# Kernel optimization log

Hardware: AMD Instinct MI355X
Metric: run time of the kernel (lower is better)

The kernel has to match this reference:

```python
import jax, jax.numpy as jnp
import numpy as np

MEM_DIM = 1024
N_CHILD = 16384

def _linear_params(key, out_dim, in_dim):
    kw, kb = jax.random.split(key)
    bound = 1.0 / np.sqrt(in_dim)
    W = jax.random.uniform(kw, (out_dim, in_dim), jnp.float32, -bound, bound)
    b = jax.random.uniform(kb, (out_dim,), jnp.float32, -bound, bound)
    return W, b

def setup_inputs() -> dict:
    key = jax.random.key(0)
    ks = jax.random.split(key, 7)
    child_c = jax.random.normal(ks[0], (N_CHILD, MEM_DIM), jnp.float32)
    child_h = jax.random.normal(ks[1], (N_CHILD, MEM_DIM), jnp.float32)
    child_h_sum = jax.random.normal(ks[2], (MEM_DIM,), jnp.float32)
    W_ih, b_ih = _linear_params(ks[3], MEM_DIM, MEM_DIM)
    W_fh, b_fh = _linear_params(ks[4], MEM_DIM, MEM_DIM)
    W_uh, b_uh = _linear_params(ks[5], MEM_DIM, MEM_DIM)
    W_oh, b_oh = _linear_params(ks[6], MEM_DIM, MEM_DIM)
    return {
        "child_c": child_c, "child_h": child_h, "child_h_sum": child_h_sum,
        "W_ih": W_ih, "b_ih": b_ih, "W_fh": W_fh, "b_fh": b_fh,
        "W_uh": W_uh, "b_uh": b_uh, "W_oh": W_oh, "b_oh": b_oh,
    }

def reference(child_c, child_h, child_h_sum,
              W_ih, b_ih, W_fh, b_fh, W_uh, b_uh, W_oh, b_oh):
    # Gate projections on the summed child hidden state: [mem_dim]
    i = jax.nn.sigmoid(child_h_sum @ W_ih.T + b_ih)
    o = jax.nn.sigmoid(child_h_sum @ W_oh.T + b_oh)
    u = jnp.tanh(child_h_sum @ W_uh.T + b_uh)
    # Per-child forget gates, batched (replaces the Python loop): [N, mem_dim]
    f = jax.nn.sigmoid(child_h @ W_fh.T + b_fh)
    fc = f * child_c                     # [N, mem_dim]
    c = i * u + jnp.sum(fc, axis=0)      # [mem_dim]
    h = o * jnp.tanh(c)                  # [mem_dim]
    return (c, h)
```

## Files before the change

### kernel.cpp

```cpp
#include <hip/hip_runtime.h>
#include <hip/hip_bf16.h>
#include <math.h>

#define MEM_DIM 1024
#define N_CHILD 16384

#define BM 128
#define BN 64
#define BK 128
#define KITERS (MEM_DIM / BK)

typedef __bf16 bf16_t;
typedef __bf16 bf16x4 __attribute__((ext_vector_type(4)));
typedef __bf16 bf16x8 __attribute__((ext_vector_type(8)));
typedef float f32x4 __attribute__((ext_vector_type(4)));

__device__ __forceinline__ void async_load16(const bf16_t* g, bf16_t* l) {
    __builtin_amdgcn_global_load_lds(
        (const __attribute__((address_space(1))) unsigned int*)g,
        (__attribute__((address_space(3))) unsigned int*)l,
        16, 0, 0);
}

__global__ __launch_bounds__(256) void prep_kernel(
        const float* __restrict__ child_h, const float* __restrict__ W_fh,
        bf16_t* __restrict__ dst, int n8,
        const float* __restrict__ hsum,
        const float* __restrict__ W_ih, const float* __restrict__ b_ih,
        const float* __restrict__ W_uh, const float* __restrict__ b_uh,
        const float* __restrict__ W_oh, const float* __restrict__ b_oh,
        float* __restrict__ acc_c, float* __restrict__ o_ws) {
    const int tid = threadIdx.x;
    if (blockIdx.x < MEM_DIM) {
        const int j = blockIdx.x;
        const float* wi = W_ih + (size_t)j * MEM_DIM;
        const float* wu = W_uh + (size_t)j * MEM_DIM;
        const float* wo = W_oh + (size_t)j * MEM_DIM;
        float si = 0.f, su = 0.f, so = 0.f;
        for (int k = tid; k < MEM_DIM; k += 256) {
            float hv = hsum[k];
            si += wi[k] * hv;
            su += wu[k] * hv;
            so += wo[k] * hv;
        }
        for (int off = 32; off > 0; off >>= 1) {
            si += __shfl_down(si, off, 64);
            su += __shfl_down(su, off, 64);
            so += __shfl_down(so, off, 64);
        }
        __shared__ float red[3][4];
        const int wave = tid >> 6, lane = tid & 63;
        if (lane == 0) { red[0][wave] = si; red[1][wave] = su; red[2][wave] = so; }
        __syncthreads();
        if (tid == 0) {
            float ti = red[0][0] + red[0][1] + red[0][2] + red[0][3] + b_ih[j];
            float tu = red[1][0] + red[1][1] + red[1][2] + red[1][3] + b_uh[j];
            float to = red[2][0] + red[2][1] + red[2][2] + red[2][3] + b_oh[j];
            float iv = 1.f / (1.f + expf(-ti));
            float uv = tanhf(tu);
            float ov = 1.f / (1.f + expf(-to));
            acc_c[j] = iv * uv;
            o_ws[j]  = ov;
        }
    } else {
        const int nA8 = (N_CHILD * MEM_DIM) / 8;
        int t = (blockIdx.x - MEM_DIM) * 256 + tid;
        if (t < n8) {
            const float* s = (t < nA8) ? (child_h + (size_t)t * 8)
                                       : (W_fh + (size_t)(t - nA8) * 8);
            float4 a = *(const float4*)s;
            float4 b = *(const float4*)(s + 4);
            bf16x8 o = { (bf16_t)a.x, (bf16_t)a.y, (bf16_t)a.z, (bf16_t)a.w,
                         (bf16_t)b.x, (bf16_t)b.y, (bf16_t)b.z, (bf16_t)b.w };
            *(bf16x8*)(dst + (size_t)t * 8) = o;
        }
    }
}

__global__ __launch_bounds__(256) void fused_gemm_bf16(
        const bf16_t* __restrict__ hbf, const bf16_t* __restrict__ wbf,
        const float* __restrict__ child_c, const float* __restrict__ b_fh,
        float* __restrict__ acc_c) {
    __shared__ __align__(1024) bf16_t sA[BM * BK];
    __shared__ __align__(1024) bf16_t sB[BN * BK];
    __shared__ float sred[BN];

    const int tid  = threadIdx.x;
    const int lane = tid & 63;
    const int wave = tid >> 6;
    const int wr = wave >> 1;
    const int wc = wave & 1;
    const int q  = lane >> 4;
    const int cl = lane & 15;

    const int b   = blockIdx.x;
    const int xcd = b & 7;
    const int l   = b >> 3;
    const int jt  = l & 15;
    const int ntl = l >> 4;
    const int j0  = jt * BN;
    const int n0  = (xcd * 16 + ntl) * BM;

    const int rl = lane >> 4;
    const int p  = lane & 15;
    const bf16_t* gA[8];
    bf16_t* lA[8];
#pragma unroll
    for (int i = 0; i < 8; i++) {
        const int r = wave * 32 + i * 4 + rl;
        const int cg = p ^ (r & 15);
        gA[i] = hbf + (size_t)(n0 + r) * MEM_DIM + cg * 8;
        lA[i] = &sA[(wave * 32 + i * 4) * BK];
    }
    const bf16_t* gB[4];
    bf16_t* lB[4];
#pragma unroll
    for (int i = 0; i < 4; i++) {
        const int r = wave * 16 + i * 4 + rl;
        const int cg = p ^ (r & 15);
        gB[i] = wbf + (size_t)(j0 + r) * MEM_DIM + cg * 8;
        lB[i] = &sB[(wave * 16 + i * 4) * BK];
    }

    f32x4 acc[4][2];
#pragma unroll
    for (int a = 0; a < 4; a++)
#pragma unroll
        for (int c = 0; c < 2; c++) acc[a][c] = (f32x4)0.0f;

    for (int k = 0; k < KITERS; ++k) {
#pragma unroll
        for (int i = 0; i < 8; i++) { async_load16(gA[i], lA[i]); gA[i] += BK; }
#pragma unroll
        for (int i = 0; i < 4; i++) { async_load16(gB[i], lB[i]); gB[i] += BK; }
        __syncthreads();

#pragma unroll
        for (int h = 0; h < 4; h++) {
            bf16x8 af[4], bfr[2];
#pragma unroll
            for (int mt = 0; mt < 4; mt++) {
                const int ra = wr * 64 + mt * 16 + cl;
                af[mt] = *(const bf16x8*)(&sA[ra * BK + (((4 * h + q) ^ (ra & 15)) * 8)]);
            }
#pragma unroll
            for (int nt = 0; nt < 2; nt++) {
                const int rb = wc * 32 + nt * 16 + cl;
                bfr[nt] = *(const bf16x8*)(&sB[rb * BK + (((4 * h + q) ^ (rb & 15)) * 8)]);
            }
#pragma unroll
            for (int mt = 0; mt < 4; mt++)
#pragma unroll
                for (int nt = 0; nt < 2; nt++)
                    acc[mt][nt] = __builtin_amdgcn_mfma_f32_16x16x32_bf16(
                        af[mt], bfr[nt], acc[mt][nt], 0, 0, 0);
        }
        __syncthreads();
    }

    if (tid < BN) sred[tid] = 0.0f;
    __syncthreads();

    float colsum[2] = {0.f, 0.f};
#pragma unroll
    for (int nt = 0; nt < 2; nt++) {
        const int col = j0 + wc * 32 + nt * 16 + cl;
        const float bias = b_fh[col];
#pragma unroll
        for (int mt = 0; mt < 4; mt++) {
#pragma unroll
            for (int r = 0; r < 4; r++) {
                const int row = n0 + wr * 64 + mt * 16 + q * 4 + r;
                float s = acc[mt][nt][r] + bias;
                float fg = 1.0f / (1.0f + __expf(-s));
                colsum[nt] += fg * child_c[(size_t)row * MEM_DIM + col];
            }
        }
        colsum[nt] += __shfl_xor(colsum[nt], 16, 64);
        colsum[nt] += __shfl_xor(colsum[nt], 32, 64);
    }
    if (q == 0) {
#pragma unroll
        for (int nt = 0; nt < 2; nt++)
            atomicAdd(&sred[wc * 32 + nt * 16 + cl], colsum[nt]);
    }
    __syncthreads();
    if (tid < BN) atomicAdd(&acc_c[j0 + tid], sred[tid]);
}

__global__ void finalize_kernel(const float* __restrict__ acc_c,
                                const float* __restrict__ o_ws,
                                float* __restrict__ out) {
    int t = blockIdx.x * 256 + threadIdx.x;
    if (t < MEM_DIM) {
        float cv = acc_c[t];
        float hv = o_ws[t] * tanhf(cv);
        out[t] = cv;
        out[MEM_DIM + t] = hv;
    }
}

__global__ void gates_kernel(const float* __restrict__ hsum,
                             const float* __restrict__ W_ih, const float* __restrict__ b_ih,
                             const float* __restrict__ W_uh, const float* __restrict__ b_uh,
                             const float* __restrict__ W_oh, const float* __restrict__ b_oh,
                             float* __restrict__ acc_c, float* __restrict__ o_ws) {
    const int j = blockIdx.x;
    const int tid = threadIdx.x;
    const float* wi = W_ih + (size_t)j * MEM_DIM;
    const float* wu = W_uh + (size_t)j * MEM_DIM;
    const float* wo = W_oh + (size_t)j * MEM_DIM;
    float si = 0.f, su = 0.f, so = 0.f;
    for (int k = tid; k < MEM_DIM; k += 256) {
        float hv = hsum[k];
        si += wi[k] * hv;
        su += wu[k] * hv;
        so += wo[k] * hv;
    }
    for (int off = 32; off > 0; off >>= 1) {
        si += __shfl_down(si, off, 64);
        su += __shfl_down(su, off, 64);
        so += __shfl_down(so, off, 64);
    }
    __shared__ float red[3][4];
    const int wave = tid >> 6, lane = tid & 63;
    if (lane == 0) { red[0][wave] = si; red[1][wave] = su; red[2][wave] = so; }
    __syncthreads();
    if (tid == 0) {
        float ti = red[0][0] + red[0][1] + red[0][2] + red[0][3] + b_ih[j];
        float tu = red[1][0] + red[1][1] + red[1][2] + red[1][3] + b_uh[j];
        float to = red[2][0] + red[2][1] + red[2][2] + red[2][3] + b_oh[j];
        acc_c[j] = (1.f / (1.f + expf(-ti))) * tanhf(tu);
        o_ws[j]  = 1.f / (1.f + expf(-to));
    }
}

#define LDS_STRIDE 40
__global__ __launch_bounds__(256) void fused_gemm_f32(
        const float* __restrict__ child_h, const float* __restrict__ child_c,
        const float* __restrict__ W_fh, const float* __restrict__ b_fh,
        float* __restrict__ acc_c) {
    __shared__ __align__(16) bf16_t sA[128 * LDS_STRIDE];
    __shared__ __align__(16) bf16_t sB[128 * LDS_STRIDE];
    __shared__ float sred[128];
    const int tid = threadIdx.x, lane = tid & 63, wave = tid >> 6;
    const int wr = wave >> 1, wc = wave & 1;
    const int j0 = blockIdx.x * 128, n0 = blockIdx.y * 128;
    const int q = lane >> 4, cl = lane & 15;
    f32x4 acc[4][4];
#pragma unroll
    for (int a = 0; a < 4; a++)
#pragma unroll
        for (int c = 0; c < 4; c++) acc[a][c] = (f32x4)0.0f;
    for (int k0 = 0; k0 < MEM_DIM; k0 += 32) {
#pragma unroll
        for (int i = 0; i < 4; i++) {
            int f = tid + i * 256, row = f >> 3, col = (f & 7) * 4;
            float4 va = *(const float4*)(child_h + (size_t)(n0 + row) * MEM_DIM + k0 + col);
            float4 vb = *(const float4*)(W_fh    + (size_t)(j0 + row) * MEM_DIM + k0 + col);
            bf16x4 ba = { (bf16_t)va.x, (bf16_t)va.y, (bf16_t)va.z, (bf16_t)va.w };
            bf16x4 bb = { (bf16_t)vb.x, (bf16_t)vb.y, (bf16_t)vb.z, (bf16_t)vb.w };
            *(bf16x4*)(&sA[row * LDS_STRIDE + col]) = ba;
            *(bf16x4*)(&sB[row * LDS_STRIDE + col]) = bb;
        }
        __syncthreads();
        bf16x8 af[4], bfr[4];
#pragma unroll
        for (int mt = 0; mt < 4; mt++) {
            af[mt]  = *(const bf16x8*)(&sA[(wr * 64 + mt * 16 + cl) * LDS_STRIDE + q * 8]);
            bfr[mt] = *(const bf16x8*)(&sB[(wc * 64 + mt * 16 + cl) * LDS_STRIDE + q * 8]);
        }
#pragma unroll
        for (int mt = 0; mt < 4; mt++)
#pragma unroll
            for (int nt = 0; nt < 4; nt++)
                acc[mt][nt] = __builtin_amdgcn_mfma_f32_16x16x32_bf16(af[mt], bfr[nt], acc[mt][nt], 0, 0, 0);
        __syncthreads();
    }
    if (tid < 128) sred[tid] = 0.0f;
    __syncthreads();
    float colsum[4] = {0.f, 0.f, 0.f, 0.f};
#pragma unroll
    for (int nt = 0; nt < 4; nt++) {
        const int col = j0 + wc * 64 + nt * 16 + cl;
        const float bias = b_fh[col];
#pragma unroll
        for (int mt = 0; mt < 4; mt++)
#pragma unroll
            for (int r = 0; r < 4; r++) {
                const int row = n0 + wr * 64 + mt * 16 + q * 4 + r;
                float s = acc[mt][nt][r] + bias;
                float fg = 1.0f / (1.0f + __expf(-s));
                colsum[nt] += fg * child_c[(size_t)row * MEM_DIM + col];
            }
        colsum[nt] += __shfl_xor(colsum[nt], 16, 64);
        colsum[nt] += __shfl_xor(colsum[nt], 32, 64);
    }
    if (q == 0)
#pragma unroll
        for (int nt = 0; nt < 4; nt++)
            atomicAdd(&sred[wc * 64 + nt * 16 + cl], colsum[nt]);
    __syncthreads();
    if (tid < 128) atomicAdd(&acc_c[j0 + tid], sred[tid]);
}

extern "C" void kernel_launch(void* const* d_in, const int* in_sizes, int n_in,
                              void* d_out, int out_size, void* d_ws, size_t ws_size,
                              hipStream_t stream) {
    const float* child_c = (const float*)d_in[0];
    const float* child_h = (const float*)d_in[1];
    const float* hsum    = (const float*)d_in[2];
    const float* W_ih    = (const float*)d_in[3];
    const float* b_ih    = (const float*)d_in[4];
    const float* W_fh    = (const float*)d_in[5];
    const float* b_fh    = (const float*)d_in[6];
    const float* W_uh    = (const float*)d_in[7];
    const float* b_uh    = (const float*)d_in[8];
    const float* W_oh    = (const float*)d_in[9];
    const float* b_oh    = (const float*)d_in[10];
    float* out   = (float*)d_out;

    float* acc_c = (float*)d_ws;
    float* o_ws  = acc_c + MEM_DIM;
    const size_t HBF_OFF   = 8192;
    const size_t HBF_BYTES = (size_t)N_CHILD * MEM_DIM * 2;
    const size_t WBF_BYTES = (size_t)MEM_DIM * MEM_DIM * 2;
    const size_t NEED = HBF_OFF + HBF_BYTES + WBF_BYTES;

    if (ws_size >= NEED) {
        bf16_t* hbf = (bf16_t*)((char*)d_ws + HBF_OFF);
        bf16_t* wbf = hbf + (size_t)N_CHILD * MEM_DIM;
        const int n8 = (N_CHILD * MEM_DIM + MEM_DIM * MEM_DIM) / 8;
        const int cvtBlocks = (n8 + 255) / 256;
        prep_kernel<<<MEM_DIM + cvtBlocks, 256, 0, stream>>>(
            child_h, W_fh, hbf, n8,
            hsum, W_ih, b_ih, W_uh, b_uh, W_oh, b_oh, acc_c, o_ws);
        fused_gemm_bf16<<<(N_CHILD / BM) * (MEM_DIM / BN), 256, 0, stream>>>(
            hbf, wbf, child_c, b_fh, acc_c);
    } else {
        gates_kernel<<<MEM_DIM, 256, 0, stream>>>(hsum, W_ih, b_ih, W_uh, b_uh,
                                                  W_oh, b_oh, acc_c, o_ws);
        dim3 grid(MEM_DIM / 128, N_CHILD / 128);
        fused_gemm_f32<<<grid, 256, 0, stream>>>(child_h, child_c, W_fh, b_fh, acc_c);
    }
    finalize_kernel<<<(MEM_DIM + 255) / 256, 256, 0, stream>>>(acc_c, o_ws, out);
}
```

Before: 215.4 us.

## Halve GEMM K-tile, raise occupancy, and prefetch child_c into registers before main loop

Cuts the K tile from 128 to 64, which halves LDS use per block, and adds a launch bound asking for 4 blocks per CU. The async load mapping and XOR swizzle are redone for the narrower 64-element rows. The child_c values and bias needed by the epilogue are now loaded into registers before the K loop, so their global latency can overlap the GEMM instead of stalling the epilogue. The trade-off is 32 extra live registers per thread under a tighter register cap, which risks spills, plus twice as many K iterations and barriers.

```diff
diff --git a/kernel.cpp b/kernel.cpp
--- a/kernel.cpp
+++ b/kernel.cpp
@@ -7,7 +7,7 @@
 
 #define BM 128
 #define BN 64
-#define BK 128
+#define BK 64
 #define KITERS (MEM_DIM / BK)
 
 typedef __bf16 bf16_t;
@@ -77,7 +77,7 @@
     }
 }
 
-__global__ __launch_bounds__(256) void fused_gemm_bf16(
+__global__ __launch_bounds__(256, 4) void fused_gemm_bf16(
         const bf16_t* __restrict__ hbf, const bf16_t* __restrict__ wbf,
         const float* __restrict__ child_c, const float* __restrict__ b_fh,
         float* __restrict__ acc_c) {
@@ -101,25 +101,24 @@
     const int j0  = jt * BN;
     const int n0  = (xcd * 16 + ntl) * BM;
 
-    const int rl = lane >> 4;
-    const int p  = lane & 15;
-    const bf16_t* gA[8];
-    bf16_t* lA[8];
-#pragma unroll
-    for (int i = 0; i < 8; i++) {
-        const int r = wave * 32 + i * 4 + rl;
-        const int cg = p ^ (r & 15);
-        gA[i] = hbf + (size_t)(n0 + r) * MEM_DIM + cg * 8;
-        lA[i] = &sA[(wave * 32 + i * 4) * BK];
-    }
-    const bf16_t* gB[4];
-    bf16_t* lB[4];
+    const int rl = lane >> 3;
+    const int p  = lane & 7;
+    const int cf = (p ^ rl) * 8;
+    const bf16_t* gA[4];
+    bf16_t* lA[4];
 #pragma unroll
     for (int i = 0; i < 4; i++) {
-        const int r = wave * 16 + i * 4 + rl;
-        const int cg = p ^ (r & 15);
-        gB[i] = wbf + (size_t)(j0 + r) * MEM_DIM + cg * 8;
-        lB[i] = &sB[(wave * 16 + i * 4) * BK];
+        const int r = wave * 32 + i * 8 + rl;
+        gA[i] = hbf + (size_t)(n0 + r) * MEM_DIM + cf;
+        lA[i] = &sA[(wave * 32 + i * 8) * BK];
+    }
+    const bf16_t* gB[2];
+    bf16_t* lB[2];
+#pragma unroll
+    for (int i = 0; i < 2; i++) {
+        const int r = wave * 16 + i * 8 + rl;
+        gB[i] = wbf + (size_t)(j0 + r) * MEM_DIM + cf;
+        lB[i] = &sB[(wave * 16 + i * 8) * BK];
     }
 
     f32x4 acc[4][2];
@@ -128,25 +127,41 @@
 #pragma unroll
         for (int c = 0; c < 2; c++) acc[a][c] = (f32x4)0.0f;
 
+    float ccr[2][4][4];
+    float biasr[2];
+    {
+        const float* ccp = child_c + (size_t)(n0 + wr * 64 + q * 4) * MEM_DIM
+                                   + j0 + wc * 32 + cl;
+#pragma unroll
+        for (int nt = 0; nt < 2; nt++) {
+            biasr[nt] = b_fh[j0 + wc * 32 + nt * 16 + cl];
+#pragma unroll
+            for (int mt = 0; mt < 4; mt++)
+#pragma unroll
+                for (int r = 0; r < 4; r++)
+                    ccr[nt][mt][r] = ccp[(size_t)(mt * 16 + r) * MEM_DIM + nt * 16];
+        }
+    }
+
     for (int k = 0; k < KITERS; ++k) {
 #pragma unroll
-        for (int i = 0; i < 8; i++) { async_load16(gA[i], lA[i]); gA[i] += BK; }
-#pragma unroll
-        for (int i = 0; i < 4; i++) { async_load16(gB[i], lB[i]); gB[i] += BK; }
-        __syncthreads();
-
-#pragma unroll
-        for (int h = 0; h < 4; h++) {
+        for (int i = 0; i < 4; i++) { async_load16(gA[i], lA[i]); gA[i] += BK; }
+#pragma unroll
+        for (int i = 0; i < 2; i++) { async_load16(gB[i], lB[i]); gB[i] += BK; }
+        __syncthreads();
+
+#pragma unroll
+        for (int h = 0; h < 2; h++) {
             bf16x8 af[4], bfr[2];
 #pragma unroll
             for (int mt = 0; mt < 4; mt++) {
                 const int ra = wr * 64 + mt * 16 + cl;
-                af[mt] = *(const bf16x8*)(&sA[ra * BK + (((4 * h + q) ^ (ra & 15)) * 8)]);
+                af[mt] = *(const bf16x8*)(&sA[ra * BK + (((4 * h + q) ^ (cl & 7)) * 8)]);
             }
 #pragma unroll
             for (int nt = 0; nt < 2; nt++) {
                 const int rb = wc * 32 + nt * 16 + cl;
-                bfr[nt] = *(const bf16x8*)(&sB[rb * BK + (((4 * h + q) ^ (rb & 15)) * 8)]);
+                bfr[nt] = *(const bf16x8*)(&sB[rb * BK + (((4 * h + q) ^ (cl & 7)) * 8)]);
             }
 #pragma unroll
             for (int mt = 0; mt < 4; mt++)
@@ -164,16 +179,13 @@
     float colsum[2] = {0.f, 0.f};
 #pragma unroll
     for (int nt = 0; nt < 2; nt++) {
-        const int col = j0 + wc * 32 + nt * 16 + cl;
-        const float bias = b_fh[col];
 #pragma unroll
         for (int mt = 0; mt < 4; mt++) {
 #pragma unroll
             for (int r = 0; r < 4; r++) {
-                const int row = n0 + wr * 64 + mt * 16 + q * 4 + r;
-                float s = acc[mt][nt][r] + bias;
+                float s = acc[mt][nt][r] + biasr[nt];
                 float fg = 1.0f / (1.0f + __expf(-s));
-                colsum[nt] += fg * child_c[(size_t)row * MEM_DIM + col];
+                colsum[nt] += fg * ccr[nt][mt][r];
             }
         }
         colsum[nt] += __shfl_xor(colsum[nt], 16, 64);
```

Result: slower. 228.4 us (+6.0%).
